# Performance work log

Measured on AMD Instinct MI355X. Metric: run time of the kernel, lower is better.

Reference implementation:

```python
import jax, jax.numpy as jnp
import numpy as np

NUM_CLASSES = 22
SKIP = 20            # skip_pixels: stride over flattened pixel index
N_STEPS = 200        # discretized steps along each voting ray
STEP = 4.0           # pixels per ray step
INLIER_T = 0.9       # inlier_threshold on direction dot-product
LABEL_T = 500.0      # label_threshold: min #pixels of a class to be valid


def _hough_forward(label_2d, vertex_pred, extents, poses, meta_data):
    B, H, W = label_2d.shape
    C = NUM_CLASSES
    HW = H * W

    # ---- strided pixel sampling (skip_pixels) ----
    idx = jnp.arange(0, HW, SKIP)                      # [P]
    P = idx.shape[0]
    ys = (idx // W).astype(jnp.float32)                # [P]
    xs = (idx % W).astype(jnp.float32)
    labels = label_2d.reshape(B, HW)[:, idx].astype(jnp.int32)   # [B,P]
    vp = vertex_pred.reshape(B, HW, C, 3)[:, idx]                # [B,P,C,3]
    # pick each pixel's predicted (dx,dy,z) for its own class label
    sel = jnp.take_along_axis(
        vp, jnp.broadcast_to(labels[:, :, None, None], (B, P, 1, 3)), axis=2
    )[:, :, 0]                                                   # [B,P,3]
    d = sel[..., :2]
    dn = d / (jnp.linalg.norm(d, axis=-1, keepdims=True) + 1e-9)  # unit dir [B,P,2]
    z = sel[..., 2]                                               # [B,P]
    fg = labels > 0                                               # foreground mask

    # ---- ray voting into per-class Hough accumulator ----
    t = (jnp.arange(N_STEPS, dtype=jnp.float32) + 1.0) * STEP     # [T]
    cx = xs[None, :, None] + dn[..., 0:1] * t[None, None, :]      # [B,P,T]
    cy = ys[None, :, None] + dn[..., 1:2] * t[None, None, :]
    cxi = jnp.round(cx).astype(jnp.int32)
    cyi = jnp.round(cy).astype(jnp.int32)
    inb = (cxi >= 0) & (cxi < W) & (cyi >= 0) & (cyi < H) & fg[..., None]
    cxi = jnp.clip(cxi, 0, W - 1)
    cyi = jnp.clip(cyi, 0, H - 1)
    bidx = jnp.arange(B, dtype=jnp.int32)[:, None, None]
    flat = ((bidx * C + labels[:, :, None]) * H + cyi) * W + cxi  # [B,P,T]
    hough = jnp.zeros((B * C * HW,), jnp.float32)
    hough = hough.at[flat.reshape(-1)].add(inb.reshape(-1).astype(jnp.float32))
    hough = hough.reshape(B, C, H, W)

    # ---- per-class peak ----
    hflat = hough.reshape(B, C, HW)
    vmax = hflat.max(-1)                               # [B,C]
    pk = jnp.argmax(hflat, axis=-1).astype(jnp.int32)  # [B,C]
    pky = (pk // W).astype(jnp.float32)
    pkx = (pk % W).astype(jnp.float32)

    # ---- validity: enough labeled pixels for the class ----
    b2 = jnp.arange(B, dtype=jnp.int32)[:, None]
    counts = jnp.zeros((B, C), jnp.float32).at[
        jnp.broadcast_to(b2, (B, HW)).reshape(-1),
        label_2d.reshape(-1).astype(jnp.int32),
    ].add(1.0)                                          # [B,C] full-res pixel counts
    cls_ids = jnp.arange(C, dtype=jnp.float32)
    valid = (counts >= LABEL_T) & (cls_ids[None, :] > 0)  # [B,C]

    # ---- inlier selection + inlier-averaged depth ----
    cx_c = jnp.take_along_axis(pkx, labels, axis=1)    # [B,P] peak of pixel's class
    cy_c = jnp.take_along_axis(pky, labels, axis=1)
    dvec = jnp.stack([cx_c - xs[None, :], cy_c - ys[None, :]], axis=-1)
    dvec = dvec / (jnp.linalg.norm(dvec, axis=-1, keepdims=True) + 1e-9)
    dot = jnp.sum(dn * dvec, axis=-1)                  # [B,P]
    inl = (fg & (dot > INLIER_T)).astype(jnp.float32)  # [B,P]
    bP = jnp.broadcast_to(b2, (B, P)).reshape(-1)
    z_sum = jnp.zeros((B, C), jnp.float32).at[bP, labels.reshape(-1)].add((z * inl).reshape(-1))
    n_inl = jnp.zeros((B, C), jnp.float32).at[bP, labels.reshape(-1)].add(inl.reshape(-1))
    depth = z_sum / jnp.maximum(n_inl, 1.0)            # [B,C]
    z_safe = jnp.where(jnp.abs(depth) > 1e-3, depth, 1.0)

    # ---- bbox from extents + intrinsics ----
    fx = meta_data[:, 0:1]                             # [B,1]
    fy = meta_data[:, 4:5]
    diam = jnp.linalg.norm(extents, axis=-1)[None, :]  # [1,C]
    half_w = 0.5 * diam * fx / z_safe
    half_h = 0.5 * diam * fy / z_safe
    vmask = valid.astype(jnp.float32)
    rois = jnp.stack([
        jnp.broadcast_to(b2.astype(jnp.float32), (B, C)),
        jnp.broadcast_to(cls_ids[None, :], (B, C)),
        pkx - half_w, pky - half_h, pkx + half_w, pky + half_h,
        vmax,
    ], axis=-1) * vmask[..., None]                     # [B,C,7]

    # ---- pose init: identity quaternion + backprojected translation ----
    Kinv = meta_data[:, 9:18].reshape(B, 3, 3)
    hom = jnp.stack([pkx, pky, jnp.ones_like(pkx)], axis=-1)      # [B,C,3]
    ray = jnp.einsum('bij,bcj->bci', Kinv, hom)
    T = depth[..., None] * ray                                    # [B,C,3]
    quat = jnp.broadcast_to(jnp.array([1.0, 0.0, 0.0, 0.0], jnp.float32), (B, C, 4))
    pose_out = jnp.concatenate([quat, T], axis=-1) * vmask[..., None]  # [B,C,7]

    return jnp.concatenate([rois, pose_out], axis=-1)  # [B,C,14]


def setup_inputs() -> dict:
    key = jax.random.key(0)
    k1, k2, k3 = jax.random.split(key, 3)
    B, H, W = 2, 480, 640
    label_2d = jax.random.randint(k1, (B, H, W), 0, NUM_CLASSES, dtype=jnp.int32)
    vertex_pred = jax.random.normal(k2, (B, H, W, 3 * NUM_CLASSES), dtype=jnp.float32)
    extents = jax.random.uniform(k3, (NUM_CLASSES, 3), minval=0.05, maxval=0.3, dtype=jnp.float32)
    poses = jnp.zeros((B, 13), jnp.float32)
    K = np.array([[1066.778, 0, 312.9869], [0, 1067.487, 241.3109], [0, 0, 1]], dtype=np.float32)
    Kinv = np.linalg.pinv(K).astype(np.float32)
    md = np.zeros((B, 48), np.float32)
    md[:, 0:9] = K.flatten()
    md[:, 9:18] = Kinv.flatten()
    meta_data = jnp.asarray(md)
    return {"label_2d": label_2d, "vertex_pred": vertex_pred, "extents": extents,
            "poses": poses, "meta_data": meta_data}


def reference(label_2d, vertex_pred, extents, poses, meta_data):
    return _hough_forward(label_2d, vertex_pred, extents, poses, meta_data)
```

## Files before the change

kernel.cpp:

```cpp
#include <hip/hip_runtime.h>
#include <math.h>

#define C_      22
#define SKIP_   20
#define NSTEP_  200
#define STEP_   4.0f
#define INL_T_  0.9f
#define LAB_T_  500
#define B_      2
#define H_      480
#define W_      640
#define HW_     (H_ * W_)
#define P_      (HW_ / SKIP_)

#define TS_       64
#define TILES_X_  (W_ / TS_)
#define NTILES_Y_ 8
#define NTILES_   (TILES_X_ * NTILES_Y_)
#define NPLANES_  (B_ * (C_ - 1))
#define NPT_      (NPLANES_ * NTILES_)
#define CAP_      2048

#define SUB_A_    8
#define SEG_LEN_  (NSTEP_ / SUB_A_)
#define PA_BLOCKS_    ((B_ * P_ * SUB_A_) / 256)
#define COUNT_BLOCKS_ ((B_ * HW_) / 256)
#define INL_BLOCKS_   ((B_ * P_) / 256)

#define KEY_INIT_ 0x00000000FFFFFFFFull

__device__ __forceinline__ void emit_run(unsigned int* cnt, uint4* lists, int pt,
                                         int xi, int yi, int i0, int i1,
                                         float dnx, float dny) {
    unsigned slot = atomicAdd(&cnt[pt], 1u);
    if (slot < CAP_) {
        uint4 r;
        r.x = (unsigned)xi | ((unsigned)yi << 16);
        r.y = (unsigned)i0 | ((unsigned)i1 << 8);
        r.z = __float_as_uint(dnx);
        r.w = __float_as_uint(dny);
        lists[(size_t)pt * CAP_ + slot] = r;
    }
}

__global__ __launch_bounds__(256) void binray_count_kernel(const int* __restrict__ label,
                                                           const float* __restrict__ vp,
                                                           unsigned int* __restrict__ cnt,
                                                           uint4* __restrict__ lists,
                                                           int* __restrict__ counts,
                                                           unsigned long long* __restrict__ key) {
    if (blockIdx.x < PA_BLOCKS_) {
        int tid = blockIdx.x * 256 + threadIdx.x;
        int pt  = tid >> 3;
        int sub = tid & 7;
        int b   = pt / P_;
        int pi  = pt - b * P_;
        int idx = pi * SKIP_;
        int lab = label[b * HW_ + idx];
        if (lab <= 0) return;
        int xi = idx % W_, yi = idx / W_;
        float xs = (float)xi, ys = (float)yi;
        const float* s = vp + ((size_t)(b * HW_ + idx) * (C_ * 3)) + lab * 3;
        float dx = s[0], dy = s[1];
        float nrm = sqrtf(__fadd_rn(__fmul_rn(dx, dx), __fmul_rn(dy, dy))) + 1e-9f;
        float dnx = dx / nrm, dny = dy / nrm;
        int base = (b * (C_ - 1) + (lab - 1)) * NTILES_;
        int curTile = -1, runStart = 0;
        bool entered = false;
        int iBeg = sub * SEG_LEN_, iEnd = iBeg + SEG_LEN_;
        for (int i = iBeg; i < iEnd; ++i) {
            float t = (float)(i + 1) * STEP_;
            float cx = __fadd_rn(xs, __fmul_rn(dnx, t));
            float cy = __fadd_rn(ys, __fmul_rn(dny, t));
            float cxr = rintf(cx);
            float cyr = rintf(cy);
            int tl2 = -1;
            if (cxr >= 0.0f && cxr <= (float)(W_ - 1) && cyr >= 0.0f && cyr <= (float)(H_ - 1))
                tl2 = (((int)cyr) >> 6) * TILES_X_ + (((int)cxr) >> 6);
            if (tl2 != curTile) {
                if (curTile >= 0)
                    emit_run(cnt, lists, base + curTile, xi, yi, runStart, i - 1, dnx, dny);
                curTile = tl2;
                runStart = i;
            }
            if (tl2 >= 0) entered = true;
            else if (entered) break;
        }
        if (curTile >= 0)
            emit_run(cnt, lists, base + curTile, xi, yi, runStart, iEnd - 1, dnx, dny);
    } else {
        __shared__ int h[C_];
        int cb  = blockIdx.x - PA_BLOCKS_;
        if (cb == 0 && threadIdx.x < B_ * C_)
            key[threadIdx.x] = KEY_INIT_;
        const int bpb = HW_ / 256;
        int b   = cb / bpb;
        int off = (cb % bpb) * 256 + threadIdx.x;
        if (threadIdx.x < C_) h[threadIdx.x] = 0;
        __syncthreads();
        int lab = label[b * HW_ + off];
        atomicAdd(&h[lab], 1);
        __syncthreads();
        if (threadIdx.x < C_) {
            int v = h[threadIdx.x];
            if (v) atomicAdd(&counts[b * C_ + threadIdx.x], v);
        }
    }
}

__global__ __launch_bounds__(256) void raster_argmax_kernel(const unsigned int* __restrict__ cnt,
                                                            const uint4* __restrict__ lists,
                                                            unsigned long long* __restrict__ key) {
    __shared__ unsigned int tile[TS_ * TS_ / 2];
    __shared__ unsigned int sv[256];
    __shared__ int          si[256];
    int pt = blockIdx.x;
    int n = (int)cnt[pt];
    if (n == 0) return;
    if (n > CAP_) n = CAP_;
    {
        uint4* t4 = (uint4*)tile;
        t4[threadIdx.x]       = make_uint4(0u, 0u, 0u, 0u);
        t4[threadIdx.x + 256] = make_uint4(0u, 0u, 0u, 0u);
    }
    __syncthreads();
    int p  = pt / NTILES_;
    int tl = pt % NTILES_;
    int b = p / (C_ - 1);
    int c = p % (C_ - 1) + 1;
    int x0 = (tl % TILES_X_) * TS_;
    int y0 = (tl / TILES_X_) * TS_;
    const uint4* lst = lists + (size_t)pt * CAP_;
    int hwv = threadIdx.x >> 5, ln = threadIdx.x & 31;
    for (int r = hwv; r < n; r += 8) {
        uint4 rec = lst[r];
        int i0 = (int)(rec.y & 0xFFu), i1 = (int)((rec.y >> 8) & 0xFFu);
        float xs = (float)(rec.x & 0xFFFFu);
        float ys = (float)(rec.x >> 16);
        float dnx = __uint_as_float(rec.z);
        float dny = __uint_as_float(rec.w);
        for (int i = i0 + ln; i <= i1; i += 32) {
            float t = (float)(i + 1) * STEP_;
            float cx = __fadd_rn(xs, __fmul_rn(dnx, t));
            float cy = __fadd_rn(ys, __fmul_rn(dny, t));
            int lx = (int)rintf(cx) - x0;
            int ly = (int)rintf(cy) - y0;
            int cell = ly * TS_ + lx;
            atomicAdd(&tile[cell >> 1], 1u << ((cell & 1) * 16));
        }
    }
    __syncthreads();
    unsigned bv = 0u; int bi = 0;
    {
        unsigned w0 = tile[threadIdx.x];
        bv = w0 & 0xFFFFu; bi = threadIdx.x * 2;
        unsigned hi = w0 >> 16;
        if (hi > bv) { bv = hi; bi = threadIdx.x * 2 + 1; }
    }
    #pragma unroll
    for (int j = 1; j < 8; ++j) {
        int ix = threadIdx.x + j * 256;
        unsigned w = tile[ix];
        unsigned lo = w & 0xFFFFu, hi = w >> 16;
        if (lo > bv) { bv = lo; bi = ix * 2; }
        if (hi > bv) { bv = hi; bi = ix * 2 + 1; }
    }
    sv[threadIdx.x] = bv; si[threadIdx.x] = bi;
    __syncthreads();
    for (int s = 128; s > 0; s >>= 1) {
        if (threadIdx.x < s) {
            unsigned ov = sv[threadIdx.x + s]; int oi = si[threadIdx.x + s];
            if (ov > sv[threadIdx.x] || (ov == sv[threadIdx.x] && oi < si[threadIdx.x])) {
                sv[threadIdx.x] = ov; si[threadIdx.x] = oi;
            }
        }
        __syncthreads();
    }
    if (threadIdx.x == 0) {
        int ly = si[0] >> 6, lx = si[0] & 63;
        unsigned gidx = (unsigned)((y0 + ly) * W_ + (x0 + lx));
        unsigned long long k = ((unsigned long long)sv[0] << 32)
                             | (unsigned long long)(0xFFFFFFFFu - gidx);
        atomicMax(&key[b * C_ + c], k);
    }
}

__global__ __launch_bounds__(256) void inlier_kernel(const int* __restrict__ label,
                                                     const float* __restrict__ vp,
                                                     const unsigned long long* __restrict__ key,
                                                     float* __restrict__ z_sum,
                                                     float* __restrict__ n_inl) {
    __shared__ float zs[C_];
    __shared__ float ns[C_];
    const int bpb = P_ / 256;
    int b  = blockIdx.x / bpb;
    int pi = (blockIdx.x % bpb) * 256 + threadIdx.x;
    if (threadIdx.x < C_) { zs[threadIdx.x] = 0.0f; ns[threadIdx.x] = 0.0f; }
    __syncthreads();
    int idx = pi * SKIP_;
    int lab = label[b * HW_ + idx];
    if (lab > 0) {
        float ys = (float)(idx / W_);
        float xs = (float)(idx % W_);
        const float* s = vp + ((size_t)(b * HW_ + idx) * (C_ * 3)) + lab * 3;
        float dx = s[0], dy = s[1], z = s[2];
        float nrm = sqrtf(__fadd_rn(__fmul_rn(dx, dx), __fmul_rn(dy, dy))) + 1e-9f;
        float dnx = dx / nrm, dny = dy / nrm;
        unsigned long long k = key[b * C_ + lab];
        int pkv = (int)(0xFFFFFFFFu - (unsigned int)(k & 0xFFFFFFFFull));
        float pkx = (float)(pkv % W_), pky = (float)(pkv / W_);
        float dvx = __fsub_rn(pkx, xs), dvy = __fsub_rn(pky, ys);
        float nrm2 = sqrtf(__fadd_rn(__fmul_rn(dvx, dvx), __fmul_rn(dvy, dvy))) + 1e-9f;
        dvx /= nrm2; dvy /= nrm2;
        float dot = __fadd_rn(__fmul_rn(dnx, dvx), __fmul_rn(dny, dvy));
        if (dot > INL_T_) {
            atomicAdd(&zs[lab], z);
            atomicAdd(&ns[lab], 1.0f);
        }
    }
    __syncthreads();
    if (threadIdx.x < C_) {
        if (ns[threadIdx.x] != 0.0f) {
            atomicAdd(&z_sum[b * C_ + threadIdx.x], zs[threadIdx.x]);
            atomicAdd(&n_inl[b * C_ + threadIdx.x], ns[threadIdx.x]);
        }
    }
}

__global__ __launch_bounds__(64) void finalize_kernel(const int* __restrict__ counts,
                                                      const unsigned long long* __restrict__ key,
                                                      const float* __restrict__ z_sum,
                                                      const float* __restrict__ n_inl,
                                                      const float* __restrict__ extents,
                                                      const float* __restrict__ meta,
                                                      float* __restrict__ out) {
    int t = threadIdx.x;
    if (t >= B_ * C_) return;
    int b = t / C_, c = t % C_;
    float* o = out + t * 14;
    bool valid = (counts[t] >= LAB_T_) && (c > 0);
    if (!valid) {
        #pragma unroll
        for (int k2 = 0; k2 < 14; ++k2) o[k2] = 0.0f;
        return;
    }
    float depth = z_sum[t] / fmaxf(n_inl[t], 1.0f);
    float z_safe = (fabsf(depth) > 0.001f) ? depth : 1.0f;
    float fx = meta[b * 48 + 0];
    float fy = meta[b * 48 + 4];
    const float* e = extents + c * 3;
    float diam = sqrtf(e[0]*e[0] + e[1]*e[1] + e[2]*e[2]);
    unsigned long long k = key[t];
    float vmax = (float)(unsigned int)(k >> 32);
    int pkv = (int)(0xFFFFFFFFu - (unsigned int)(k & 0xFFFFFFFFull));
    float pkx = (float)(pkv % W_), pky = (float)(pkv / W_);
    float half_w = ((0.5f * diam) * fx) / z_safe;
    float half_h = ((0.5f * diam) * fy) / z_safe;
    o[0] = (float)b;
    o[1] = (float)c;
    o[2] = pkx - half_w;
    o[3] = pky - half_h;
    o[4] = pkx + half_w;
    o[5] = pky + half_h;
    o[6] = vmax;
    const float* Ki = meta + b * 48 + 9;
    float rx = Ki[0]*pkx + Ki[1]*pky + Ki[2];
    float ry = Ki[3]*pkx + Ki[4]*pky + Ki[5];
    float rz = Ki[6]*pkx + Ki[7]*pky + Ki[8];
    o[7]  = 1.0f;
    o[8]  = 0.0f;
    o[9]  = 0.0f;
    o[10] = 0.0f;
    o[11] = depth * rx;
    o[12] = depth * ry;
    o[13] = depth * rz;
}

extern "C" void kernel_launch(void* const* d_in, const int* in_sizes, int n_in,
                              void* d_out, int out_size, void* d_ws, size_t ws_size,
                              hipStream_t stream) {
    const int*   label   = (const int*)d_in[0];
    const float* vp      = (const float*)d_in[1];
    const float* extents = (const float*)d_in[2];
    const float* meta    = (const float*)d_in[4];
    float* out = (float*)d_out;

    char* ws = (char*)d_ws;
    size_t off = 0;
    unsigned int* cnt = (unsigned int*)(ws + off);  off += NPT_ * sizeof(unsigned int);
    int*   counts = (int*)(ws + off);   off += B_ * C_ * sizeof(int);
    float* z_sum  = (float*)(ws + off); off += B_ * C_ * sizeof(float);
    float* n_inl  = (float*)(ws + off); off += B_ * C_ * sizeof(float);
    size_t zero_bytes = off;
    off = (off + 15) & ~(size_t)15;
    unsigned long long* key = (unsigned long long*)(ws + off);
    off += B_ * C_ * sizeof(unsigned long long);
    off = (off + 15) & ~(size_t)15;
    uint4* lists = (uint4*)(ws + off);

    hipMemsetAsync(d_ws, 0, zero_bytes, stream);

    binray_count_kernel<<<PA_BLOCKS_ + COUNT_BLOCKS_, 256, 0, stream>>>(label, vp, cnt, lists, counts, key);
    raster_argmax_kernel<<<NPT_, 256, 0, stream>>>(cnt, lists, key);
    inlier_kernel<<<INL_BLOCKS_, 256, 0, stream>>>(label, vp, key, z_sum, n_inl);
    finalize_kernel<<<1, 64, 0, stream>>>(counts, key, z_sum, n_inl, extents, meta, out);
}
```

Baseline: 270.8 us.

## Fuse pipeline into one cooperative persistent kernel with grid syncs

Replaces the memset plus four separate kernel launches with a single cooperative kernel of 512 persistent blocks. The stages (zeroing, ray binning and label counting, tile rasterization and argmax, inlier accumulation, finalize) are separated by grid.sync(). The aim is to remove launch and inter-kernel gaps. In exchange, parallelism is capped at 512 blocks with grid-stride loops, the finalize stage runs on one block while others idle, and each grid barrier has its own cost. The old multi-kernel path is kept as a fallback when cooperative launch is unsupported or fails.

```diff
diff --git a/kernel.cpp b/kernel.cpp
--- a/kernel.cpp
+++ b/kernel.cpp
@@ -1,5 +1,8 @@
 #include <hip/hip_runtime.h>
+#include <hip/hip_cooperative_groups.h>
 #include <math.h>
+
+namespace cg = cooperative_groups;
 
 #define C_      22
 #define SKIP_   20
@@ -27,6 +30,8 @@
 #define COUNT_BLOCKS_ ((B_ * HW_) / 256)
 #define INL_BLOCKS_   ((B_ * P_) / 256)
 
+#define GRID_     512
+
 #define KEY_INIT_ 0x00000000FFFFFFFFull
 
 __device__ __forceinline__ void emit_run(unsigned int* cnt, uint4* lists, int pt,
@@ -43,6 +48,241 @@
     }
 }
 
+__global__ __launch_bounds__(256, 2) void hough_mega_kernel(
+        const int* __restrict__ label, const float* __restrict__ vp,
+        const float* __restrict__ extents, const float* __restrict__ meta,
+        float* __restrict__ out,
+        unsigned int* __restrict__ cnt, int* __restrict__ counts,
+        float* __restrict__ z_sum, float* __restrict__ n_inl,
+        unsigned long long* __restrict__ key, uint4* __restrict__ lists) {
+    cg::grid_group grid = cg::this_grid();
+    __shared__ union {
+        struct { unsigned int tile[TS_ * TS_ / 2]; unsigned int sv[256]; int si[256]; } rb;
+        struct { int h[C_]; float zs[C_]; float ns[C_]; } hs;
+    } sm;
+    const int tid = threadIdx.x;
+    const int gtid = blockIdx.x * 256 + tid;
+
+    for (int i = gtid; i < NPT_; i += GRID_ * 256) cnt[i] = 0u;
+    if (gtid < B_ * C_) {
+        counts[gtid] = 0;
+        z_sum[gtid] = 0.0f;
+        n_inl[gtid] = 0.0f;
+        key[gtid] = KEY_INIT_;
+    }
+    grid.sync();
+
+    for (int u = blockIdx.x; u < PA_BLOCKS_ + COUNT_BLOCKS_; u += GRID_) {
+        if (u < PA_BLOCKS_) {
+            int t0  = u * 256 + tid;
+            int pt  = t0 >> 3;
+            int sub = t0 & 7;
+            int b   = pt / P_;
+            int pi  = pt - b * P_;
+            int idx = pi * SKIP_;
+            int lab = label[b * HW_ + idx];
+            if (lab > 0) {
+                int xi = idx % W_, yi = idx / W_;
+                float xs = (float)xi, ys = (float)yi;
+                const float* s = vp + ((size_t)(b * HW_ + idx) * (C_ * 3)) + lab * 3;
+                float dx = s[0], dy = s[1];
+                float nrm = sqrtf(__fadd_rn(__fmul_rn(dx, dx), __fmul_rn(dy, dy))) + 1e-9f;
+                float dnx = dx / nrm, dny = dy / nrm;
+                int base = (b * (C_ - 1) + (lab - 1)) * NTILES_;
+                int curTile = -1, runStart = 0;
+                bool entered = false;
+                int iBeg = sub * SEG_LEN_, iEnd = iBeg + SEG_LEN_;
+                for (int i = iBeg; i < iEnd; ++i) {
+                    float t = (float)(i + 1) * STEP_;
+                    float cx = __fadd_rn(xs, __fmul_rn(dnx, t));
+                    float cy = __fadd_rn(ys, __fmul_rn(dny, t));
+                    float cxr = rintf(cx);
+                    float cyr = rintf(cy);
+                    int tl2 = -1;
+                    if (cxr >= 0.0f && cxr <= (float)(W_ - 1) && cyr >= 0.0f && cyr <= (float)(H_ - 1))
+                        tl2 = (((int)cyr) >> 6) * TILES_X_ + (((int)cxr) >> 6);
+                    if (tl2 != curTile) {
+                        if (curTile >= 0)
+                            emit_run(cnt, lists, base + curTile, xi, yi, runStart, i - 1, dnx, dny);
+                        curTile = tl2;
+                        runStart = i;
+                    }
+                    if (tl2 >= 0) entered = true;
+                    else if (entered) break;
+                }
+                if (curTile >= 0)
+                    emit_run(cnt, lists, base + curTile, xi, yi, runStart, iEnd - 1, dnx, dny);
+            }
+        } else {
+            int cb = u - PA_BLOCKS_;
+            const int bpb = HW_ / 256;
+            int b   = cb / bpb;
+            int off = (cb % bpb) * 256 + tid;
+            if (tid < C_) sm.hs.h[tid] = 0;
+            __syncthreads();
+            int lab = label[b * HW_ + off];
+            atomicAdd(&sm.hs.h[lab], 1);
+            __syncthreads();
+            if (tid < C_) {
+                int v = sm.hs.h[tid];
+                if (v) atomicAdd(&counts[b * C_ + tid], v);
+            }
+        }
+    }
+    grid.sync();
+
+    for (int pt = blockIdx.x; pt < NPT_; pt += GRID_) {
+        int n = (int)cnt[pt];
+        if (n == 0) continue;
+        if (n > CAP_) n = CAP_;
+        {
+            uint4* t4 = (uint4*)sm.rb.tile;
+            t4[tid]       = make_uint4(0u, 0u, 0u, 0u);
+            t4[tid + 256] = make_uint4(0u, 0u, 0u, 0u);
+        }
+        __syncthreads();
+        int p  = pt / NTILES_;
+        int tl = pt % NTILES_;
+        int b = p / (C_ - 1);
+        int c = p % (C_ - 1) + 1;
+        int x0 = (tl % TILES_X_) * TS_;
+        int y0 = (tl / TILES_X_) * TS_;
+        const uint4* lst = lists + (size_t)pt * CAP_;
+        int hwv = tid >> 5, ln = tid & 31;
+        for (int r = hwv; r < n; r += 8) {
+            uint4 rec = lst[r];
+            int i0 = (int)(rec.y & 0xFFu), i1 = (int)((rec.y >> 8) & 0xFFu);
+            float xs = (float)(rec.x & 0xFFFFu);
+            float ys = (float)(rec.x >> 16);
+            float dnx = __uint_as_float(rec.z);
+            float dny = __uint_as_float(rec.w);
+            for (int i = i0 + ln; i <= i1; i += 32) {
+                float t = (float)(i + 1) * STEP_;
+                float cx = __fadd_rn(xs, __fmul_rn(dnx, t));
+                float cy = __fadd_rn(ys, __fmul_rn(dny, t));
+                int lx = (int)rintf(cx) - x0;
+                int ly = (int)rintf(cy) - y0;
+                int cell = ly * TS_ + lx;
+                atomicAdd(&sm.rb.tile[cell >> 1], 1u << ((cell & 1) * 16));
+            }
+        }
+        __syncthreads();
+        unsigned bv = 0u; int bi = 0;
+        {
+            unsigned w0 = sm.rb.tile[tid];
+            bv = w0 & 0xFFFFu; bi = tid * 2;
+            unsigned hi = w0 >> 16;
+            if (hi > bv) { bv = hi; bi = tid * 2 + 1; }
+        }
+        #pragma unroll
+        for (int j = 1; j < 8; ++j) {
+            int ix = tid + j * 256;
+            unsigned w = sm.rb.tile[ix];
+            unsigned lo = w & 0xFFFFu, hi = w >> 16;
+            if (lo > bv) { bv = lo; bi = ix * 2; }
+            if (hi > bv) { bv = hi; bi = ix * 2 + 1; }
+        }
+        sm.rb.sv[tid] = bv; sm.rb.si[tid] = bi;
+        __syncthreads();
+        for (int s = 128; s > 0; s >>= 1) {
+            if (tid < s) {
+                unsigned ov = sm.rb.sv[tid + s]; int oi = sm.rb.si[tid + s];
+                if (ov > sm.rb.sv[tid] || (ov == sm.rb.sv[tid] && oi < sm.rb.si[tid])) {
+                    sm.rb.sv[tid] = ov; sm.rb.si[tid] = oi;
+                }
+            }
+            __syncthreads();
+        }
+        if (tid == 0) {
+            int ly = sm.rb.si[0] >> 6, lx = sm.rb.si[0] & 63;
+            unsigned gidx = (unsigned)((y0 + ly) * W_ + (x0 + lx));
+            unsigned long long k = ((unsigned long long)sm.rb.sv[0] << 32)
+                                 | (unsigned long long)(0xFFFFFFFFu - gidx);
+            atomicMax(&key[b * C_ + c], k);
+        }
+    }
+    grid.sync();
+
+    if (blockIdx.x < INL_BLOCKS_) {
+        const int bpb = P_ / 256;
+        int b  = blockIdx.x / bpb;
+        int pi = (blockIdx.x % bpb) * 256 + tid;
+        if (tid < C_) { sm.hs.zs[tid] = 0.0f; sm.hs.ns[tid] = 0.0f; }
+        __syncthreads();
+        int idx = pi * SKIP_;
+        int lab = label[b * HW_ + idx];
+        if (lab > 0) {
+            float ys = (float)(idx / W_);
+            float xs = (float)(idx % W_);
+            const float* s = vp + ((size_t)(b * HW_ + idx) * (C_ * 3)) + lab * 3;
+            float dx = s[0], dy = s[1], z = s[2];
+            float nrm = sqrtf(__fadd_rn(__fmul_rn(dx, dx), __fmul_rn(dy, dy))) + 1e-9f;
+            float dnx = dx / nrm, dny = dy / nrm;
+            unsigned long long k = key[b * C_ + lab];
+            int pkv = (int)(0xFFFFFFFFu - (unsigned int)(k & 0xFFFFFFFFull));
+            float pkx = (float)(pkv % W_), pky = (float)(pkv / W_);
+            float dvx = __fsub_rn(pkx, xs), dvy = __fsub_rn(pky, ys);
+            float nrm2 = sqrtf(__fadd_rn(__fmul_rn(dvx, dvx), __fmul_rn(dvy, dvy))) + 1e-9f;
+            dvx /= nrm2; dvy /= nrm2;
+            float dot = __fadd_rn(__fmul_rn(dnx, dvx), __fmul_rn(dny, dvy));
+            if (dot > INL_T_) {
+                atomicAdd(&sm.hs.zs[lab], z);
+                atomicAdd(&sm.hs.ns[lab], 1.0f);
+            }
+        }
+        __syncthreads();
+        if (tid < C_) {
+            if (sm.hs.ns[tid] != 0.0f) {
+                atomicAdd(&z_sum[b * C_ + tid], sm.hs.zs[tid]);
+                atomicAdd(&n_inl[b * C_ + tid], sm.hs.ns[tid]);
+            }
+        }
+    }
+    grid.sync();
+
+    if (blockIdx.x == 0 && tid < B_ * C_) {
+        int t = tid;
+        int b = t / C_, c = t % C_;
+        float* o = out + t * 14;
+        bool valid = (counts[t] >= LAB_T_) && (c > 0);
+        if (!valid) {
+            #pragma unroll
+            for (int k2 = 0; k2 < 14; ++k2) o[k2] = 0.0f;
+        } else {
+            float depth = z_sum[t] / fmaxf(n_inl[t], 1.0f);
+            float z_safe = (fabsf(depth) > 0.001f) ? depth : 1.0f;
+            float fx = meta[b * 48 + 0];
+            float fy = meta[b * 48 + 4];
+            const float* e = extents + c * 3;
+            float diam = sqrtf(e[0]*e[0] + e[1]*e[1] + e[2]*e[2]);
+            unsigned long long k = key[t];
+            float vmax = (float)(unsigned int)(k >> 32);
+            int pkv = (int)(0xFFFFFFFFu - (unsigned int)(k & 0xFFFFFFFFull));
+            float pkx = (float)(pkv % W_), pky = (float)(pkv / W_);
+            float half_w = ((0.5f * diam) * fx) / z_safe;
+            float half_h = ((0.5f * diam) * fy) / z_safe;
+            o[0] = (float)b;
+            o[1] = (float)c;
+            o[2] = pkx - half_w;
+            o[3] = pky - half_h;
+            o[4] = pkx + half_w;
+            o[5] = pky + half_h;
+            o[6] = vmax;
+            const float* Ki = meta + b * 48 + 9;
+            float rx = Ki[0]*pkx + Ki[1]*pky + Ki[2];
+            float ry = Ki[3]*pkx + Ki[4]*pky + Ki[5];
+            float rz = Ki[6]*pkx + Ki[7]*pky + Ki[8];
+            o[7]  = 1.0f;
+            o[8]  = 0.0f;
+            o[9]  = 0.0f;
+            o[10] = 0.0f;
+            o[11] = depth * rx;
+            o[12] = depth * ry;
+            o[13] = depth * rz;
+        }
+    }
+}
+
 __global__ __launch_bounds__(256) void binray_count_kernel(const int* __restrict__ label,
                                                            const float* __restrict__ vp,
                                                            unsigned int* __restrict__ cnt,
@@ -50,9 +290,9 @@
                                                            int* __restrict__ counts,
                                                            unsigned long long* __restrict__ key) {
     if (blockIdx.x < PA_BLOCKS_) {
-        int tid = blockIdx.x * 256 + threadIdx.x;
-        int pt  = tid >> 3;
-        int sub = tid & 7;
+        int t0  = blockIdx.x * 256 + threadIdx.x;
+        int pt  = t0 >> 3;
+        int sub = t0 & 7;
         int b   = pt / P_;
         int pi  = pt - b * P_;
         int idx = pi * SKIP_;
@@ -298,8 +538,26 @@
     off = (off + 15) & ~(size_t)15;
     uint4* lists = (uint4*)(ws + off);
 
+    static int coop = -1;
+    if (coop < 0) {
+        int dev = 0;
+        (void)hipGetDevice(&dev);
+        int v = 0;
+        (void)hipDeviceGetAttribute(&v, hipDeviceAttributeCooperativeLaunch, dev);
+        coop = v ? 1 : 0;
+    }
+
+    if (coop) {
+        void* args[] = { (void*)&label, (void*)&vp, (void*)&extents, (void*)&meta,
+                         (void*)&out, (void*)&cnt, (void*)&counts, (void*)&z_sum,
+                         (void*)&n_inl, (void*)&key, (void*)&lists };
+        hipError_t e = hipLaunchCooperativeKernel((const void*)hough_mega_kernel,
+                                                  dim3(GRID_), dim3(256), args, 0, stream);
+        if (e == hipSuccess) return;
+        coop = 0;
+    }
+
     hipMemsetAsync(d_ws, 0, zero_bytes, stream);
-
     binray_count_kernel<<<PA_BLOCKS_ + COUNT_BLOCKS_, 256, 0, stream>>>(label, vp, cnt, lists, counts, key);
     raster_argmax_kernel<<<NPT_, 256, 0, stream>>>(cnt, lists, key);
     inlier_kernel<<<INL_BLOCKS_, 256, 0, stream>>>(label, vp, key, z_sum, n_inl);
```

New measurement: 486.5 us. 79.7% more time.
